# Kernel optimization log

Measured on AMD Instinct MI355X. Metric: run time of the kernel, lower is better.

The kernel has to match this reference:

```python
import jax, jax.numpy as jnp
import numpy as np

R = 2          # candidate_radius
TEMP = 0.1     # temperature
MIN_E = 3
MAX_E = 8      # max_edges_per_node
EPS = 1e-6


def _neighbors(H, W, r):
    # grid neighbor indices (N,K) and relative positions (K,2), clamped at borders
    ys, xs = np.meshgrid(np.arange(H), np.arange(W), indexing='ij')
    idx_grid = ys * W + xs
    nbrs, rel = [], []
    for dy in range(-r, r + 1):
        for dx in range(-r, r + 1):
            if dy == 0 and dx == 0:
                continue
            ny = np.clip(ys + dy, 0, H - 1)
            nx = np.clip(xs + dx, 0, W - 1)
            nbrs.append(idx_grid[ny, nx].ravel())
            rel.append([dx / r, dy / r])
    return jnp.asarray(np.stack(nbrs, 1)), jnp.asarray(np.array(rel, np.float32))


def setup_inputs() -> dict:
    key = jax.random.key(0)
    ks = jax.random.split(key, 12)
    B, C, H, W = 2, 64, 128, 128
    hid = 64
    ein = 2 * C + 2  # edge scorer input dim
    s = 0.05
    return {
        'x':  jax.random.normal(ks[0], (B, C, H, W), jnp.float32),
        'W1': jax.random.normal(ks[1], (hid, ein), jnp.float32) * s,
        'b1': jnp.zeros((hid,), jnp.float32),
        'W2': jax.random.normal(ks[2], (hid // 2, hid), jnp.float32) * s,
        'b2': jnp.zeros((hid // 2,), jnp.float32),
        'W3': jax.random.normal(ks[3], (1, hid // 2), jnp.float32) * s,
        'b3': jnp.zeros((1,), jnp.float32),
        'thr': jnp.asarray(0.0, jnp.float32),
        'Wm': jax.random.normal(ks[4], (C, C), jnp.float32) * s,
        'bm': jnp.zeros((C,), jnp.float32),
        'Wo': jax.random.normal(ks[5], (C, C), jnp.float32) * s,
        'bo': jnp.zeros((C,), jnp.float32),
    }


def reference(x, W1, b1, W2, b2, W3, b3, thr, Wm, bm, Wo, bo):
    B, C, H, W = x.shape
    N = H * W
    nbr, rel = _neighbors(H, W, R)          # (N,K), (K,2)
    K = nbr.shape[1]

    nodes = x.transpose(0, 2, 3, 1).reshape(B, N, C)   # (B,N,C)
    h_tgt = jnp.take(nodes, nbr, axis=1)               # (B,N,K,C) gather neighbors

    # edge scorer layer1: split W1 over [h_src | h_tgt | rel_pos] to avoid (B,N,K,2C+2) concat
    z_src = nodes @ W1[:, :C].T                        # (B,N,hid)
    z_tgt = h_tgt @ W1[:, C:2 * C].T                   # (B,N,K,hid)
    z_pos = rel @ W1[:, 2 * C:].T                      # (K,hid)
    h1 = jax.nn.relu(z_src[:, :, None, :] + z_tgt + z_pos[None, None] + b1)
    h2 = jax.nn.relu(h1 @ W2.T + b2)
    edge_scores = jax.nn.sigmoid((h2 @ W3.T + b3)[..., 0])   # (B,N,K)

    thr_v = jax.nn.sigmoid(thr)
    keep_prob = jax.nn.sigmoid((edge_scores - thr_v) / TEMP)
    mask_thr = edge_scores >= thr_v
    counts = mask_thr.sum(axis=2)                       # (B,N)

    def topk_mask(k):
        _, idx = jax.lax.top_k(edge_scores, k)          # (B,N,k)
        return jax.nn.one_hot(idx, K, dtype=jnp.float32).sum(-2) > 0

    m_max = topk_mask(min(MAX_E, K))
    m_min = topk_mask(min(MIN_E, K))
    use_max = (counts > MAX_E)[..., None]
    use_min = (counts < MIN_E)[..., None]
    use_t = ~use_max & ~use_min
    final_mask = (use_max & m_max) | (use_min & m_min) | (use_t & mask_thr)

    msgs = jax.nn.relu(h_tgt @ Wm.T + bm)               # (B,N,K,C)
    w = (edge_scores * keep_prob * final_mask.astype(edge_scores.dtype))[..., None]
    agg = (msgs * w).sum(axis=2) / (w.sum(axis=2) + EPS)  # (B,N,C)

    out = nodes + agg @ Wo.T + bo
    return out.reshape(B, H, W, C).transpose(0, 3, 1, 2)
```

## Files before the change

### kernel.cpp

```cpp
#include <hip/hip_runtime.h>
#include <hip/hip_bf16.h>
#include <math.h>

#define NNODES 16384
#define KE 24

typedef float f32x4 __attribute__((ext_vector_type(4)));
typedef unsigned u32x4 __attribute__((ext_vector_type(4)));
typedef __fp16 half2_t __attribute__((ext_vector_type(2)));
typedef _Float16 half8_t __attribute__((ext_vector_type(8)));

union fragcast { u32x4 u; half8_t h; half2_t h2[4]; };

__global__ __launch_bounds__(256) void precompute_k(
    const float* __restrict__ x, const float* __restrict__ W1,
    const float* __restrict__ Wm, const float* __restrict__ b1,
    const float* __restrict__ bm,
    float* __restrict__ zsrc, float* __restrict__ ztgt, float* __restrict__ msg,
    float* __restrict__ zpos)
{
    __shared__ float xt[64][128];
    __shared__ float wl[64][64];
    const int t = threadIdx.x;
    const int mat = blockIdx.x >> 8;
    const int tile = blockIdx.x & 255;
    const int n0 = tile * 128;
    const int b = n0 >> 14;
    const int nl0 = n0 & (NNODES - 1);
    const float* xb = x + (size_t)b * 64 * NNODES + nl0;

    if (blockIdx.x == 0) {
        for (int idx = t; idx < KE * 64; idx += 256) {
            int k = idx >> 6, h = idx & 63;
            int kk = k + (k >= 12 ? 1 : 0);
            int q5 = (kk * 52) >> 8;
            int dy = q5 - 2, dx = kk - 5 * q5 - 2;
            zpos[idx] = W1[h * 130 + 128] * (dx * 0.5f)
                      + W1[h * 130 + 129] * (dy * 0.5f);
        }
    }

    #pragma unroll
    for (int r = 0; r < 8; ++r) {
        int idx = r * 256 + t;
        int c = idx >> 5, j4 = idx & 31;
        float4 v = *(const float4*)(xb + (size_t)c * NNODES + j4 * 4);
        *(float4*)&xt[c][j4 * 4] = v;
    }
    #pragma unroll
    for (int r = 0; r < 16; ++r) {
        int idx = r * 256 + t;
        int c = idx >> 6, h = idx & 63;
        float v = (mat == 0) ? W1[h * 130 + c]
                : (mat == 1) ? W1[h * 130 + 64 + c]
                             : Wm[h * 64 + c];
        (&wl[0][0])[idx] = v;
    }
    __syncthreads();

    const int i = t >> 5;
    const int j = t & 31;

    float acc[8][4];
    #pragma unroll
    for (int a = 0; a < 8; ++a)
        #pragma unroll
        for (int bb = 0; bb < 4; ++bb) acc[a][bb] = 0.f;

    #pragma unroll 4
    for (int c = 0; c < 64; ++c) {
        float4 w0 = *(const float4*)&wl[c][i * 8];
        float4 w1 = *(const float4*)&wl[c][i * 8 + 4];
        float4 x0 = *(const float4*)&xt[c][j * 4];
        float wv[8] = {w0.x, w0.y, w0.z, w0.w, w1.x, w1.y, w1.z, w1.w};
        float xv[4] = {x0.x, x0.y, x0.z, x0.w};
        #pragma unroll
        for (int a = 0; a < 8; ++a)
            #pragma unroll
            for (int bb = 0; bb < 4; ++bb)
                acc[a][bb] = fmaf(wv[a], xv[bb], acc[a][bb]);
    }

    #pragma unroll
    for (int a = 0; a < 8; ++a) {
        float bv = (mat == 0) ? b1[i * 8 + a] : (mat == 2) ? bm[i * 8 + a] : 0.f;
        #pragma unroll
        for (int bb = 0; bb < 4; ++bb) {
            float v = acc[a][bb] + bv;
            acc[a][bb] = (mat == 2) ? fmaxf(v, 0.f) : v;
        }
    }

    float* dst = (mat == 0) ? zsrc : (mat == 1) ? ztgt : msg;
    #pragma unroll
    for (int bb = 0; bb < 4; ++bb) {
        float* o = dst + (size_t)(n0 + j * 4 + bb) * 64 + i * 8;
        *(float4*)o       = make_float4(acc[0][bb], acc[1][bb], acc[2][bb], acc[3][bb]);
        *(float4*)(o + 4) = make_float4(acc[4][bb], acc[5][bb], acc[6][bb], acc[7][bb]);
    }
}

__global__ __launch_bounds__(256, 1) void score_k(
    const float* __restrict__ zsrc, const float* __restrict__ ztgt,
    const float* __restrict__ zpos, const float* __restrict__ W2,
    const float* __restrict__ b2, const float* __restrict__ W3,
    const float* __restrict__ b3, float* __restrict__ scores)
{
    __shared__ fragcast fraglds[64 * 13];
    __shared__ float zpl[24 * 68];

    const int t = threadIdx.x;
    const int l = t & 63;
    const int lcol = l & 15;
    const int lgrp = l >> 4;
    const int w = t >> 6;
    const int wave = blockIdx.x * 4 + w;

    #pragma unroll
    for (int r = 0; r < 6; ++r) {
        int idx = r * 256 + t;
        zpl[(idx >> 6) * 68 + (idx & 63)] = zpos[idx];
    }
    {
        const int jt = w >> 1, kt = w & 1;
        fragcast fh, fl;
        const float* wr = W2 + (size_t)(jt * 16 + lcol) * 64 + kt * 32 + lgrp * 8;
        #pragma unroll
        for (int d = 0; d < 4; ++d) {
            float e0 = wr[2 * d] * 64.f;
            float e1 = wr[2 * d + 1] * 64.f;
            half2_t hh = __builtin_amdgcn_cvt_pkrtz(e0, e1);
            float r0 = e0 - (float)hh[0];
            float r1 = e1 - (float)hh[1];
            fh.h2[d] = hh;
            fl.h2[d] = __builtin_amdgcn_cvt_pkrtz(r0, r1);
        }
        fraglds[l * 13 + 0 + jt * 2 + kt] = fh;
        fraglds[l * 13 + 4 + jt * 2 + kt] = fl;
    }
    __syncthreads();

    const fragcast* fb = &fraglds[l * 13];
    const f32x4 b2l0 = *(const f32x4*)(b2 + lgrp * 4);
    const f32x4 b2l1 = *(const f32x4*)(b2 + 16 + lgrp * 4);
    const f32x4 w3l0 = *(const f32x4*)(W3 + lgrp * 4);
    const f32x4 w3l1 = *(const f32x4*)(W3 + 16 + lgrp * 4);
    const float b3s = b3[0];

    const int node0 = wave * 2;

    int kArr[3];
    float4 zsv[3][4], ztv[3][4];
    #pragma unroll
    for (int Mt = 0; Mt < 3; ++Mt) {
        const int ke = Mt * 16 + lcol;
        const int nsel = (ke >= 24) ? 1 : 0;
        const int node = node0 + nsel;
        const int k = ke - 24 * nsel;
        const int bb = node >> 14;
        const int nl = node & (NNODES - 1);
        const int yy = nl >> 7, xx = nl & 127;
        const int kk = k + (k >= 12 ? 1 : 0);
        const int q5 = (kk * 52) >> 8;
        const int dy = q5 - 2, dx = kk - 5 * q5 - 2;
        const int ny = min(max(yy + dy, 0), 127);
        const int nx = min(max(xx + dx, 0), 127);
        const int nbn = (bb << 14) + (ny << 7) + nx;
        kArr[Mt] = k;
        const float* zs = zsrc + (size_t)node * 64 + lgrp * 8;
        const float* zt = ztgt + (size_t)nbn * 64 + lgrp * 8;
        zsv[Mt][0] = *(const float4*)(zs);
        zsv[Mt][1] = *(const float4*)(zs + 4);
        zsv[Mt][2] = *(const float4*)(zs + 32);
        zsv[Mt][3] = *(const float4*)(zs + 36);
        ztv[Mt][0] = *(const float4*)(zt);
        ztv[Mt][1] = *(const float4*)(zt + 4);
        ztv[Mt][2] = *(const float4*)(zt + 32);
        ztv[Mt][3] = *(const float4*)(zt + 36);
    }

    #pragma unroll
    for (int Mt = 0; Mt < 3; ++Mt) {
        const float* zp = &zpl[kArr[Mt] * 68 + lgrp * 8];

        f32x4 ac0A = {0.f,0.f,0.f,0.f}, ac0B = {0.f,0.f,0.f,0.f};
        f32x4 ac1A = {0.f,0.f,0.f,0.f}, ac1B = {0.f,0.f,0.f,0.f};

        #pragma unroll
        for (int kt = 0; kt < 2; ++kt) {
            float4 a0 = zsv[Mt][2 * kt], a1 = zsv[Mt][2 * kt + 1];
            float4 t0 = ztv[Mt][2 * kt], t1 = ztv[Mt][2 * kt + 1];
            float4 p0 = *(const float4*)(zp + kt * 32);
            float4 p1 = *(const float4*)(zp + kt * 32 + 4);
            float v[8];
            v[0] = fmaxf(a0.x + t0.x + p0.x, 0.f);
            v[1] = fmaxf(a0.y + t0.y + p0.y, 0.f);
            v[2] = fmaxf(a0.z + t0.z + p0.z, 0.f);
            v[3] = fmaxf(a0.w + t0.w + p0.w, 0.f);
            v[4] = fmaxf(a1.x + t1.x + p1.x, 0.f);
            v[5] = fmaxf(a1.y + t1.y + p1.y, 0.f);
            v[6] = fmaxf(a1.z + t1.z + p1.z, 0.f);
            v[7] = fmaxf(a1.w + t1.w + p1.w, 0.f);

            fragcast Bh, Bl;
            #pragma unroll
            for (int d = 0; d < 4; ++d) {
                float e0 = v[2 * d], e1 = v[2 * d + 1];
                half2_t hh = __builtin_amdgcn_cvt_pkrtz(e0, e1);
                float r0 = e0 - (float)hh[0];
                float r1 = e1 - (float)hh[1];
                Bh.h2[d] = hh;
                Bl.h2[d] = __builtin_amdgcn_cvt_pkrtz(r0, r1);
            }

            ac0A = __builtin_amdgcn_mfma_f32_16x16x32_f16(fb[0 + kt].h, Bh.h, ac0A, 0, 0, 0);
            ac1A = __builtin_amdgcn_mfma_f32_16x16x32_f16(fb[2 + kt].h, Bh.h, ac1A, 0, 0, 0);
            ac0B = __builtin_amdgcn_mfma_f32_16x16x32_f16(fb[4 + kt].h, Bh.h, ac0B, 0, 0, 0);
            ac1B = __builtin_amdgcn_mfma_f32_16x16x32_f16(fb[6 + kt].h, Bh.h, ac1B, 0, 0, 0);
            ac0B = __builtin_amdgcn_mfma_f32_16x16x32_f16(fb[0 + kt].h, Bl.h, ac0B, 0, 0, 0);
            ac1B = __builtin_amdgcn_mfma_f32_16x16x32_f16(fb[2 + kt].h, Bl.h, ac1B, 0, 0, 0);
        }

        const f32x4 s0 = ac0A + ac0B;
        const f32x4 s1 = ac1A + ac1B;
        float sacc = 0.f;
        #pragma unroll
        for (int q = 0; q < 4; ++q) {
            sacc = fmaf(fmaxf(fmaf(s0[q], 0.015625f, b2l0[q]), 0.f), w3l0[q], sacc);
            sacc = fmaf(fmaxf(fmaf(s1[q], 0.015625f, b2l1[q]), 0.f), w3l1[q], sacc);
        }
        sacc += __shfl_xor(sacc, 16);
        sacc += __shfl_xor(sacc, 32);
        float sig = 1.f / (1.f + expf(-(sacc + b3s)));
        if (l < 16)
            scores[(size_t)node0 * 24 + Mt * 16 + l] = sig;
    }
}

__global__ __launch_bounds__(256) void agg_k(
    const float* __restrict__ x, const float* __restrict__ scores,
    const float* __restrict__ msg, const float* __restrict__ Wo,
    const float* __restrict__ bo, const float* __restrict__ thrp,
    float* __restrict__ out)
{
    __shared__ float sc[768];
    __shared__ float wl[768];
    __shared__ float sumw[32];
    __shared__ float aggL[32][64];
    __shared__ float ot[64][33];

    const int t = threadIdx.x;
    const int n0 = blockIdx.x * 32;
    const int b = n0 >> 14;
    const int nl0 = n0 & (NNODES - 1);
    const float thr_v = 1.f / (1.f + expf(-thrp[0]));

    #pragma unroll
    for (int rep = 0; rep < 3; ++rep)
        sc[rep * 256 + t] = scores[(size_t)n0 * 24 + rep * 256 + t];
    __syncthreads();

    #pragma unroll
    for (int rep = 0; rep < 3; ++rep) {
        int e = rep * 256 + t;
        int nl = (int)(((unsigned)(e >> 3) * 171u) >> 9);
        int k = e - nl * 24;
        float s_e = sc[e];
        int rank = 0, cnt = 0;
        #pragma unroll
        for (int j = 0; j < 24; ++j) {
            float sj = sc[nl * 24 + j];
            rank += (sj > s_e || (sj == s_e && j < k)) ? 1 : 0;
            cnt  += (sj >= thr_v) ? 1 : 0;
        }
        bool mask = (cnt > 8) ? (rank < 8)
                  : ((cnt < 3) ? (rank < 3) : (s_e >= thr_v));
        float keep = 1.f / (1.f + expf(-(s_e - thr_v) * 10.f));
        wl[e] = mask ? s_e * keep : 0.f;
    }
    __syncthreads();

    if (t < 32) {
        float s = 0.f;
        #pragma unroll
        for (int k = 0; k < 24; ++k) s += wl[t * 24 + k];
        sumw[t] = s + 1e-6f;
    }
    __syncthreads();

    const int lane = t & 63;
    const int g4 = t >> 6;

    #pragma unroll
    for (int it = 0; it < 8; ++it) {
        int nl = g4 + it * 4;
        int nn = nl0 + nl;
        int yy = nn >> 7, xx = nn & 127;
        float acc = 0.f;
        #pragma unroll
        for (int k = 0; k < 24; ++k) {
            int kk = k + (k >= 12 ? 1 : 0);
            int q5 = (kk * 52) >> 8;
            int dy = q5 - 2, dx = kk - 5 * q5 - 2;
            int ny = min(max(yy + dy, 0), 127);
            int nx = min(max(xx + dx, 0), 127);
            int nb = (b << 14) + (ny << 7) + nx;
            acc = fmaf(wl[nl * 24 + k], msg[(size_t)nb * 64 + lane], acc);
        }
        aggL[nl][lane] = acc / sumw[nl];
    }

    float4 wo[16];
    #pragma unroll
    for (int c4 = 0; c4 < 16; ++c4) wo[c4] = ((const float4*)Wo)[lane * 16 + c4];
    __syncthreads();

    #pragma unroll
    for (int it = 0; it < 8; ++it) {
        int nl = g4 + it * 4;
        const float4* ar = (const float4*)aggL[nl];
        float a0 = 0.f, a1 = 0.f, a2 = 0.f, a3 = 0.f;
        #pragma unroll
        for (int c4 = 0; c4 < 16; ++c4) {
            float4 wv = wo[c4];
            float4 av = ar[c4];
            a0 = fmaf(av.x, wv.x, a0);
            a1 = fmaf(av.y, wv.y, a1);
            a2 = fmaf(av.z, wv.z, a2);
            a3 = fmaf(av.w, wv.w, a3);
        }
        float v = (a0 + a1) + (a2 + a3) + bo[lane]
                + x[(size_t)b * 64 * NNODES + (size_t)lane * NNODES + nl0 + nl];
        ot[lane][nl] = v;
    }
    __syncthreads();

    #pragma unroll
    for (int rep = 0; rep < 2; ++rep) {
        int idx = rep * 256 + t;
        int o = idx >> 3, p = idx & 7;
        float4 v = make_float4(ot[o][4 * p + 0], ot[o][4 * p + 1],
                               ot[o][4 * p + 2], ot[o][4 * p + 3]);
        *(float4*)(out + (size_t)b * 64 * NNODES + (size_t)o * NNODES + nl0 + 4 * p) = v;
    }
}

extern "C" void kernel_launch(void* const* d_in, const int* in_sizes, int n_in,
                              void* d_out, int out_size, void* d_ws, size_t ws_size,
                              hipStream_t stream)
{
    const float* x   = (const float*)d_in[0];
    const float* W1  = (const float*)d_in[1];
    const float* b1  = (const float*)d_in[2];
    const float* W2  = (const float*)d_in[3];
    const float* b2  = (const float*)d_in[4];
    const float* W3  = (const float*)d_in[5];
    const float* b3  = (const float*)d_in[6];
    const float* thr = (const float*)d_in[7];
    const float* Wm  = (const float*)d_in[8];
    const float* bm  = (const float*)d_in[9];
    const float* Wo  = (const float*)d_in[10];
    const float* bo  = (const float*)d_in[11];
    float* out = (float*)d_out;
    float* ws  = (float*)d_ws;

    float* zsrc   = ws;
    float* ztgt   = ws + 2097152;
    float* msg    = ws + 4194304;
    float* scores = ws + 6291456;
    float* zpos   = ws + 7077888;

    hipLaunchKernelGGL(precompute_k, dim3(768), dim3(256), 0, stream,
                       x, W1, Wm, b1, bm, zsrc, ztgt, msg, zpos);
    hipLaunchKernelGGL(score_k, dim3(4096), dim3(256), 0, stream,
                       zsrc, ztgt, zpos, W2, b2, W3, b3, scores);
    hipLaunchKernelGGL(agg_k, dim3(1024), dim3(256), 0, stream,
                       x, scores, msg, Wo, bo, thr, out);
}
```

Baseline: 90.42 us.

## Use split-fp16 MFMA for precompute projections instead of scalar FMA

Replaces the scalar FMA GEMM in precompute_k with MFMA 16x16x32 f16 instructions. Both operands are split into hi/lo fp16 halves (three MFMAs per tile) so the result stays close to fp32, and weights are pre-scaled by 64 to limit fp16 underflow. Results are staged through per-wave LDS tiles so the global stores are coalesced. In exchange it adds conversion overhead and small precision changes, and x is now read with per-lane strided scalar loads instead of float4 tiles.

```diff
diff --git a/kernel.cpp b/kernel.cpp
--- a/kernel.cpp
+++ b/kernel.cpp
@@ -19,15 +19,19 @@
     float* __restrict__ zsrc, float* __restrict__ ztgt, float* __restrict__ msg,
     float* __restrict__ zpos)
 {
-    __shared__ float xt[64][128];
-    __shared__ float wl[64][64];
+    __shared__ fragcast fragA[64 * 17];
+    __shared__ float otL[4][16 * 68];
+
     const int t = threadIdx.x;
+    const int l = t & 63;
+    const int lcol = l & 15;
+    const int lgrp = l >> 4;
+    const int w = t >> 6;
     const int mat = blockIdx.x >> 8;
     const int tile = blockIdx.x & 255;
-    const int n0 = tile * 128;
-    const int b = n0 >> 14;
-    const int nl0 = n0 & (NNODES - 1);
-    const float* xb = x + (size_t)b * 64 * NNODES + nl0;
+    const int n0g = tile * 128;
+    const int b = n0g >> 14;
+    const int nl0 = n0g & (NNODES - 1);
 
     if (blockIdx.x == 0) {
         for (int idx = t; idx < KE * 64; idx += 256) {
@@ -40,63 +44,93 @@
         }
     }
 
-    #pragma unroll
-    for (int r = 0; r < 8; ++r) {
-        int idx = r * 256 + t;
-        int c = idx >> 5, j4 = idx & 31;
-        float4 v = *(const float4*)(xb + (size_t)c * NNODES + j4 * 4);
-        *(float4*)&xt[c][j4 * 4] = v;
-    }
-    #pragma unroll
-    for (int r = 0; r < 16; ++r) {
-        int idx = r * 256 + t;
-        int c = idx >> 6, h = idx & 63;
-        float v = (mat == 0) ? W1[h * 130 + c]
-                : (mat == 1) ? W1[h * 130 + 64 + c]
-                             : Wm[h * 64 + c];
-        (&wl[0][0])[idx] = v;
-    }
-    __syncthreads();
-
-    const int i = t >> 5;
-    const int j = t & 31;
-
-    float acc[8][4];
-    #pragma unroll
-    for (int a = 0; a < 8; ++a)
-        #pragma unroll
-        for (int bb = 0; bb < 4; ++bb) acc[a][bb] = 0.f;
-
-    #pragma unroll 4
-    for (int c = 0; c < 64; ++c) {
-        float4 w0 = *(const float4*)&wl[c][i * 8];
-        float4 w1 = *(const float4*)&wl[c][i * 8 + 4];
-        float4 x0 = *(const float4*)&xt[c][j * 4];
-        float wv[8] = {w0.x, w0.y, w0.z, w0.w, w1.x, w1.y, w1.z, w1.w};
-        float xv[4] = {x0.x, x0.y, x0.z, x0.w};
-        #pragma unroll
-        for (int a = 0; a < 8; ++a)
-            #pragma unroll
-            for (int bb = 0; bb < 4; ++bb)
-                acc[a][bb] = fmaf(wv[a], xv[bb], acc[a][bb]);
-    }
-
-    #pragma unroll
-    for (int a = 0; a < 8; ++a) {
-        float bv = (mat == 0) ? b1[i * 8 + a] : (mat == 2) ? bm[i * 8 + a] : 0.f;
-        #pragma unroll
-        for (int bb = 0; bb < 4; ++bb) {
-            float v = acc[a][bb] + bv;
-            acc[a][bb] = (mat == 2) ? fmaxf(v, 0.f) : v;
-        }
-    }
-
+    {
+        const int mt = w;
+        const int h = mt * 16 + lcol;
+        const float* wrow = (mat == 0) ? (W1 + (size_t)h * 130)
+                          : (mat == 1) ? (W1 + (size_t)h * 130 + 64)
+                                       : (Wm + (size_t)h * 64);
+        #pragma unroll
+        for (int kt = 0; kt < 2; ++kt) {
+            const float* wr = wrow + kt * 32 + lgrp * 8;
+            fragcast fh, fl;
+            #pragma unroll
+            for (int d = 0; d < 4; ++d) {
+                float e0 = wr[2 * d] * 64.f;
+                float e1 = wr[2 * d + 1] * 64.f;
+                half2_t hh = __builtin_amdgcn_cvt_pkrtz(e0, e1);
+                fh.h2[d] = hh;
+                fl.h2[d] = __builtin_amdgcn_cvt_pkrtz(e0 - (float)hh[0],
+                                                      e1 - (float)hh[1]);
+            }
+            fragA[l * 17 + mt * 4 + kt * 2 + 0] = fh;
+            fragA[l * 17 + mt * 4 + kt * 2 + 1] = fl;
+        }
+    }
+    __syncthreads();
+
+    float bv[4][4];
+    #pragma unroll
+    for (int mt = 0; mt < 4; ++mt)
+        #pragma unroll
+        for (int q = 0; q < 4; ++q) {
+            int h = mt * 16 + lgrp * 4 + q;
+            bv[mt][q] = (mat == 0) ? b1[h] : (mat == 2) ? bm[h] : 0.f;
+        }
+
+    const fragcast* fa = &fragA[l * 17];
+    const float* xb = x + (size_t)b * 64 * NNODES + nl0;
     float* dst = (mat == 0) ? zsrc : (mat == 1) ? ztgt : msg;
-    #pragma unroll
-    for (int bb = 0; bb < 4; ++bb) {
-        float* o = dst + (size_t)(n0 + j * 4 + bb) * 64 + i * 8;
-        *(float4*)o       = make_float4(acc[0][bb], acc[1][bb], acc[2][bb], acc[3][bb]);
-        *(float4*)(o + 4) = make_float4(acc[4][bb], acc[5][bb], acc[6][bb], acc[7][bb]);
+    float* ot = &otL[w][0];
+
+    #pragma unroll 1
+    for (int nt = 0; nt < 2; ++nt) {
+        const int nloc = w * 32 + nt * 16;
+
+        fragcast Bh[2], Bl[2];
+        #pragma unroll
+        for (int kt = 0; kt < 2; ++kt) {
+            const float* xc = xb + (size_t)(kt * 32 + lgrp * 8) * NNODES + nloc + lcol;
+            float xv[8];
+            #pragma unroll
+            for (int i = 0; i < 8; ++i) xv[i] = xc[(size_t)i * NNODES];
+            #pragma unroll
+            for (int d = 0; d < 4; ++d) {
+                half2_t hh = __builtin_amdgcn_cvt_pkrtz(xv[2 * d], xv[2 * d + 1]);
+                Bh[kt].h2[d] = hh;
+                Bl[kt].h2[d] = __builtin_amdgcn_cvt_pkrtz(xv[2 * d] - (float)hh[0],
+                                                          xv[2 * d + 1] - (float)hh[1]);
+            }
+        }
+
+        #pragma unroll
+        for (int mt = 0; mt < 4; ++mt) {
+            f32x4 acc = {0.f, 0.f, 0.f, 0.f};
+            #pragma unroll
+            for (int kt = 0; kt < 2; ++kt) {
+                fragcast Ah = fa[mt * 4 + kt * 2 + 0];
+                fragcast Al = fa[mt * 4 + kt * 2 + 1];
+                acc = __builtin_amdgcn_mfma_f32_16x16x32_f16(Ah.h, Bh[kt].h, acc, 0, 0, 0);
+                acc = __builtin_amdgcn_mfma_f32_16x16x32_f16(Al.h, Bh[kt].h, acc, 0, 0, 0);
+                acc = __builtin_amdgcn_mfma_f32_16x16x32_f16(Ah.h, Bl[kt].h, acc, 0, 0, 0);
+            }
+            #pragma unroll
+            for (int q = 0; q < 4; ++q) {
+                float v = fmaf(acc[q], 0.015625f, bv[mt][q]);
+                if (mat == 2) v = fmaxf(v, 0.f);
+                ot[lcol * 68 + mt * 16 + lgrp * 4 + q] = v;
+            }
+        }
+
+        {
+            int nn = l >> 2, qt = l & 3;
+            float* gout = dst + (size_t)(n0g + nloc + nn) * 64 + qt * 16;
+            #pragma unroll
+            for (int j = 0; j < 4; ++j) {
+                f32x4 vv = *(const f32x4*)&ot[nn * 68 + qt * 16 + j * 4];
+                *(float4*)(gout + j * 4) = make_float4(vv[0], vv[1], vv[2], vv[3]);
+            }
+        }
     }
 }
 
```

After: 84.92 us, median of 2. 1.06x faster.
